# Kernel optimization log

Hardware: AMD Instinct MI355X
Metric: run time of the kernel (lower is better)

The kernel has to match this reference:

```python
import jax, jax.numpy as jnp
import numpy as np

N, M, D = 256, 1024, 512


def setup_inputs() -> dict:
    key = jax.random.key(0)
    ks = jax.random.split(key, 12)
    s = 1.0 / np.sqrt(D)
    return {
        "q": jax.random.normal(ks[0], (N, D), jnp.float32),
        "k": jax.random.normal(ks[1], (M, D), jnp.float32),
        "v": jax.random.normal(ks[2], (M, D), jnp.float32),
        "mask": jax.random.randint(ks[3], (N, M), 0, 2, jnp.int32),
        "WQ": jax.random.normal(ks[4], (D, D), jnp.float32) * s,
        "bQ": jax.random.normal(ks[5], (D,), jnp.float32) * s,
        "WK": jax.random.normal(ks[6], (D, D), jnp.float32) * s,
        "bK": jax.random.normal(ks[7], (D,), jnp.float32) * s,
        "WV": jax.random.normal(ks[8], (D, D), jnp.float32) * s,
        "bV": jax.random.normal(ks[9], (D,), jnp.float32) * s,
        "Ww": jax.random.normal(ks[10], (1, D), jnp.float32) * s,
        "bw": jax.random.normal(ks[11], (1,), jnp.float32) * s,
    }


def reference(q, k, v, mask, WQ, bQ, WK, bK, WV, bV, Ww, bw):
    # Linear projections (torch Linear: x @ W.T + b)
    qp = q @ WQ.T + bQ            # [N, D]
    kp = k @ WK.T + bK            # [M, D]
    vp = v @ WV.T + bV            # [M, D]
    # Additive (Bahdanau) scores: tanh(q_n + k_m) . w  -> [N, M]
    t = jnp.tanh(qp[:, None, :] + kp[None, :, :])   # [N, M, D]
    score = jnp.einsum("nmd,d->nm", t, Ww[0]) + bw[0]
    score = jnp.where(mask == 1, score, jnp.float32(-1e6))
    w = jax.nn.softmax(score, axis=1)               # softmax over keys (dim 1)
    context = jnp.einsum("nm,md->nd", w, vp)        # weighted sum over keys
    return context
```

## Files before the change

### kernel.cpp

```cpp
#include <hip/hip_runtime.h>

#define NQ 256
#define MK 1024
#define DD 512
#define CSC 2.8853900817779268f
#define L2E 1.4426950408889634f

typedef __attribute__((ext_vector_type(8))) short short8;
typedef __attribute__((ext_vector_type(4))) float floatx4;

__device__ inline void bsplit(float x, unsigned short& h, unsigned short& l)
{
    unsigned u = __float_as_uint(x);
    unsigned hr = (u + 0x7FFFu + ((u >> 16) & 1u)) >> 16;
    h = (unsigned short)hr;
    float hf = __uint_as_float(hr << 16);
    unsigned ul = __float_as_uint(x - hf);
    l = (unsigned short)((ul + 0x7FFFu + ((ul >> 16) & 1u)) >> 16);
}

__global__ __launch_bounds__(256) void convert_split(
    const float* __restrict__ q, const float* __restrict__ k, const float* __restrict__ v,
    const float* __restrict__ WQ, const float* __restrict__ WK, const float* __restrict__ WV,
    unsigned short* __restrict__ qhi, unsigned short* __restrict__ qlo,
    unsigned short* __restrict__ khi, unsigned short* __restrict__ klo,
    unsigned short* __restrict__ vhi, unsigned short* __restrict__ vlo,
    unsigned short* __restrict__ wqhi, unsigned short* __restrict__ wqlo,
    unsigned short* __restrict__ wkhi, unsigned short* __restrict__ wklo,
    unsigned short* __restrict__ wvhi, unsigned short* __restrict__ wvlo)
{
    const int i = blockIdx.x * 256 + threadIdx.x;
    const float* src; unsigned short *dh, *dl; int li;
    if (i < 32768)       { src = q;  dh = qhi;  dl = qlo;  li = i; }
    else if (i < 163840) { src = k;  dh = khi;  dl = klo;  li = i - 32768; }
    else if (i < 294912) { src = v;  dh = vhi;  dl = vlo;  li = i - 163840; }
    else if (i < 360448) { src = WQ; dh = wqhi; dl = wqlo; li = i - 294912; }
    else if (i < 425984) { src = WK; dh = wkhi; dl = wklo; li = i - 360448; }
    else                 { src = WV; dh = wvhi; dl = wvlo; li = i - 425984; }

    float4 x = *(const float4*)&src[li * 4];
    ushort4 h, l;
    bsplit(x.x, h.x, l.x); bsplit(x.y, h.y, l.y);
    bsplit(x.z, h.z, l.z); bsplit(x.w, h.w, l.w);
    *(ushort4*)&dh[li * 4] = h;
    *(ushort4*)&dl[li * 4] = l;
}

__global__ __launch_bounds__(256) void proj_mfma(
    const unsigned short* __restrict__ qhi, const unsigned short* __restrict__ qlo,
    const unsigned short* __restrict__ khi, const unsigned short* __restrict__ klo,
    const unsigned short* __restrict__ vhi, const unsigned short* __restrict__ vlo,
    const unsigned short* __restrict__ wqhi, const unsigned short* __restrict__ wqlo,
    const unsigned short* __restrict__ wkhi, const unsigned short* __restrict__ wklo,
    const unsigned short* __restrict__ wvhi, const unsigned short* __restrict__ wvlo,
    const float* __restrict__ bQ, const float* __restrict__ bK, const float* __restrict__ bV,
    float* __restrict__ qs, float* __restrict__ kts, float* __restrict__ vp)
{
    int t = blockIdx.x;
    const unsigned short *Xh, *Xl, *Wh, *Wl; const float* b; int mode;
    if (t < 32)       { mode = 0; Xh = qhi; Xl = qlo; Wh = wqhi; Wl = wqlo; b = bQ; }
    else if (t < 160) { mode = 1; t -= 32;  Xh = khi; Xl = klo; Wh = wkhi; Wl = wklo; b = bK; }
    else              { mode = 2; t -= 160; Xh = vhi; Xl = vlo; Wh = wvhi; Wl = wvlo; b = bV; }
    const int i0 = (t >> 3) * 64;
    const int j0 = (t & 7) * 64;

    const int l  = threadIdx.x & 63;
    const int w  = threadIdx.x >> 6;
    const int lr = l & 15;
    const int lk = (l >> 4) * 8;
    const int rbase = (l >> 4) * 4;

    const int arow = (i0 + w * 16 + lr) * DD;

    floatx4 acc[4] = {{0,0,0,0},{0,0,0,0},{0,0,0,0},{0,0,0,0}};

    for (int kk = 0; kk < DD; kk += 32) {
        short8 ah = *(const short8*)&Xh[arow + kk + lk];
        short8 al = *(const short8*)&Xl[arow + kk + lk];
#pragma unroll
        for (int nt = 0; nt < 4; ++nt) {
            const int brow = (j0 + nt * 16 + lr) * DD;
            short8 bh = *(const short8*)&Wh[brow + kk + lk];
            short8 bl = *(const short8*)&Wl[brow + kk + lk];
            acc[nt] = __builtin_amdgcn_mfma_f32_16x16x32_bf16(ah, bh, acc[nt], 0, 0, 0);
            acc[nt] = __builtin_amdgcn_mfma_f32_16x16x32_bf16(ah, bl, acc[nt], 0, 0, 0);
            acc[nt] = __builtin_amdgcn_mfma_f32_16x16x32_bf16(al, bh, acc[nt], 0, 0, 0);
        }
    }

    if (mode == 1) {
#pragma unroll
        for (int nt = 0; nt < 4; ++nt) {
            const float bb = b[j0 + nt * 16 + lr];
            float4 o;
            o.x = (acc[nt][0] + bb) * CSC;
            o.y = (acc[nt][1] + bb) * CSC;
            o.z = (acc[nt][2] + bb) * CSC;
            o.w = (acc[nt][3] + bb) * CSC;
            *(float4*)&kts[(j0 + nt * 16 + lr) * MK + i0 + w * 16 + rbase] = o;
        }
    } else {
        float* dst = (mode == 0) ? qs : vp;
        const float sc = (mode == 0) ? CSC : 1.0f;
#pragma unroll
        for (int nt = 0; nt < 4; ++nt) {
            const float bb = b[j0 + nt * 16 + lr];
#pragma unroll
            for (int j = 0; j < 4; ++j)
                dst[(i0 + w * 16 + rbase + j) * DD + j0 + nt * 16 + lr]
                    = (acc[nt][j] + bb) * sc;
        }
    }
}

__global__ __launch_bounds__(1024) void score_sm(
    const float* __restrict__ qs, const float* __restrict__ kts,
    const float* __restrict__ Ww, const int* __restrict__ mask,
    float* __restrict__ S)
{
    const int n = blockIdx.x;
    const int t = threadIdx.x;
    const int lane = t & 63, wave = t >> 6;

    __shared__ float qsm[DD];
    __shared__ float wwm[DD];
    __shared__ float red[16];

    if (t < DD) { qsm[t] = qs[n * DD + t]; wwm[t] = Ww[t]; }
    __syncthreads();

    float acc = 0.f;
    for (int d = 0; d < DD; d += 8) {
        float kv[8];
#pragma unroll
        for (int j = 0; j < 8; ++j) kv[j] = kts[(d + j) * MK + t];
#pragma unroll
        for (int j = 0; j < 8; ++j) {
            float x = qsm[d + j] + kv[j];
            float e = __builtin_amdgcn_exp2f(x);
            acc = fmaf(wwm[d + j], __builtin_amdgcn_rcpf(e + 1.0f), acc);
        }
    }

    float s = -2.0f * acc;
    s = (mask[n * MK + t] == 1) ? s : -1e6f;

    float mx = s;
    for (int o = 32; o > 0; o >>= 1) mx = fmaxf(mx, __shfl_xor(mx, o, 64));
    if (lane == 0) red[wave] = mx;
    __syncthreads();
    if (wave == 0) {
        float r = red[lane & 15];
        for (int o = 8; o > 0; o >>= 1) r = fmaxf(r, __shfl_xor(r, o, 64));
        if (lane == 0) red[0] = r;
    }
    __syncthreads();
    mx = red[0];
    __syncthreads();

    float e = __builtin_amdgcn_exp2f((s - mx) * L2E);
    float sum = e;
    for (int o = 32; o > 0; o >>= 1) sum += __shfl_xor(sum, o, 64);
    if (lane == 0) red[wave] = sum;
    __syncthreads();
    if (wave == 0) {
        float r = red[lane & 15];
        for (int o = 8; o > 0; o >>= 1) r += __shfl_xor(r, o, 64);
        if (lane == 0) red[0] = r;
    }
    __syncthreads();
    sum = red[0];

    S[n * MK + t] = e * __builtin_amdgcn_rcpf(sum);
}

#define CNG 8
#define CMC 256

__global__ __launch_bounds__(512) void context_v2(const float* __restrict__ S,
                                                  const float* __restrict__ vp,
                                                  float* __restrict__ out)
{
    __shared__ float ws[CMC][12];
    const int t = threadIdx.x;
    const int n0 = blockIdx.x * CNG;
    const int m0 = blockIdx.y * CMC;

#pragma unroll
    for (int p = 0; p < 4; ++p) {
        int e = t + p * 512;
        int m = e & 255, n = e >> 8;
        ws[m][n] = S[(n0 + n) * MK + m0 + m];
    }
    __syncthreads();

    float acc[CNG] = {};
    for (int m = 0; m < CMC; ++m) {
        float vv = vp[(m0 + m) * DD + t];
        float4 w0 = *(const float4*)&ws[m][0];
        float4 w4 = *(const float4*)&ws[m][4];
        acc[0] = fmaf(w0.x, vv, acc[0]);
        acc[1] = fmaf(w0.y, vv, acc[1]);
        acc[2] = fmaf(w0.z, vv, acc[2]);
        acc[3] = fmaf(w0.w, vv, acc[3]);
        acc[4] = fmaf(w4.x, vv, acc[4]);
        acc[5] = fmaf(w4.y, vv, acc[5]);
        acc[6] = fmaf(w4.z, vv, acc[6]);
        acc[7] = fmaf(w4.w, vv, acc[7]);
    }
#pragma unroll
    for (int n = 0; n < CNG; ++n) atomicAdd(&out[(n0 + n) * DD + t], acc[n]);
}

extern "C" void kernel_launch(void* const* d_in, const int* in_sizes, int n_in,
                              void* d_out, int out_size, void* d_ws, size_t ws_size,
                              hipStream_t stream)
{
    const float* q    = (const float*)d_in[0];
    const float* k    = (const float*)d_in[1];
    const float* v    = (const float*)d_in[2];
    const int*   mask = (const int*)  d_in[3];
    const float* WQ   = (const float*)d_in[4];
    const float* bQ   = (const float*)d_in[5];
    const float* WK   = (const float*)d_in[6];
    const float* bK   = (const float*)d_in[7];
    const float* WV   = (const float*)d_in[8];
    const float* bV   = (const float*)d_in[9];
    const float* Ww   = (const float*)d_in[10];
    const float* bw   = (const float*)d_in[11];
    (void)bw;
    float* out = (float*)d_out;

    float* qs  = (float*)d_ws;
    float* kts = qs + NQ * DD;
    float* vp  = kts + DD * MK;
    float* S   = vp + MK * DD;
    unsigned short* p16  = (unsigned short*)(S + NQ * MK);
    unsigned short* qhi  = p16;              p16 += NQ * DD;
    unsigned short* qlo  = p16;              p16 += NQ * DD;
    unsigned short* khi  = p16;              p16 += MK * DD;
    unsigned short* klo  = p16;              p16 += MK * DD;
    unsigned short* vhi  = p16;              p16 += MK * DD;
    unsigned short* vlo  = p16;              p16 += MK * DD;
    unsigned short* wqhi = p16;              p16 += DD * DD;
    unsigned short* wqlo = p16;              p16 += DD * DD;
    unsigned short* wkhi = p16;              p16 += DD * DD;
    unsigned short* wklo = p16;              p16 += DD * DD;
    unsigned short* wvhi = p16;              p16 += DD * DD;
    unsigned short* wvlo = p16;

    hipMemsetAsync(d_out, 0, (size_t)NQ * DD * sizeof(float), stream);

    convert_split<<<1920, 256, 0, stream>>>(q, k, v, WQ, WK, WV,
        qhi, qlo, khi, klo, vhi, vlo, wqhi, wqlo, wkhi, wklo, wvhi, wvlo);

    proj_mfma<<<288, 256, 0, stream>>>(qhi, qlo, khi, klo, vhi, vlo,
        wqhi, wqlo, wkhi, wklo, wvhi, wvlo, bQ, bK, bV, qs, kts, vp);

    score_sm<<<NQ, 1024, 0, stream>>>(qs, kts, Ww, mask, S);

    context_v2<<<dim3(NQ / CNG, MK / CMC), dim3(512), 0, stream>>>(S, vp, out);
}
```

Before: 177.6 us.

## Swizzle bf16 operand layout for MFMA and block-interleave projected keys

The conversion kernel now writes the bf16 hi/lo splits in a tiled, swizzled layout. Each wave's MFMA operand fetch becomes one contiguous 16-byte-per-lane load, replacing row-strided loads. The key projection is stored as [D/8][M][8] so the score kernel reads eight d-values per thread with two float4 loads, and q and Ww are interleaved in shared memory to be read as a float2. This targets poor coalescing in the projection GEMM and the score loop, at the cost of scattered 8-byte stores in the conversion kernel and in the key-projection epilogue.

Result: faster. 158.4 us (-10.8%).

```diff
diff --git a/kernel.cpp b/kernel.cpp
--- a/kernel.cpp
+++ b/kernel.cpp
@@ -8,6 +8,12 @@
 
 typedef __attribute__((ext_vector_type(8))) short short8;
 typedef __attribute__((ext_vector_type(4))) float floatx4;
+
+__device__ inline int swz(int i, int d)
+{
+    return (((i >> 4) * 16 + (d >> 5)) << 9) | (((d >> 3) & 3) << 7)
+         | ((i & 15) << 3) | (d & 7);
+}
 
 __device__ inline void bsplit(float x, unsigned short& h, unsigned short& l)
 {
@@ -29,21 +35,24 @@
     unsigned short* __restrict__ wkhi, unsigned short* __restrict__ wklo,
     unsigned short* __restrict__ wvhi, unsigned short* __restrict__ wvlo)
 {
-    const int i = blockIdx.x * 256 + threadIdx.x;
+    const int i4 = blockIdx.x * 256 + threadIdx.x;
     const float* src; unsigned short *dh, *dl; int li;
-    if (i < 32768)       { src = q;  dh = qhi;  dl = qlo;  li = i; }
-    else if (i < 163840) { src = k;  dh = khi;  dl = klo;  li = i - 32768; }
-    else if (i < 294912) { src = v;  dh = vhi;  dl = vlo;  li = i - 163840; }
-    else if (i < 360448) { src = WQ; dh = wqhi; dl = wqlo; li = i - 294912; }
-    else if (i < 425984) { src = WK; dh = wkhi; dl = wklo; li = i - 360448; }
-    else                 { src = WV; dh = wvhi; dl = wvlo; li = i - 425984; }
+    if (i4 < 32768)       { src = q;  dh = qhi;  dl = qlo;  li = i4; }
+    else if (i4 < 163840) { src = k;  dh = khi;  dl = klo;  li = i4 - 32768; }
+    else if (i4 < 294912) { src = v;  dh = vhi;  dl = vlo;  li = i4 - 163840; }
+    else if (i4 < 360448) { src = WQ; dh = wqhi; dl = wqlo; li = i4 - 294912; }
+    else if (i4 < 425984) { src = WK; dh = wkhi; dl = wklo; li = i4 - 360448; }
+    else                  { src = WV; dh = wvhi; dl = wvlo; li = i4 - 425984; }
 
     float4 x = *(const float4*)&src[li * 4];
     ushort4 h, l;
     bsplit(x.x, h.x, l.x); bsplit(x.y, h.y, l.y);
     bsplit(x.z, h.z, l.z); bsplit(x.w, h.w, l.w);
-    *(ushort4*)&dh[li * 4] = h;
-    *(ushort4*)&dl[li * 4] = l;
+
+    const int e = li * 4;
+    const int o = swz(e >> 9, e & 511);
+    *(ushort4*)&dh[o] = h;
+    *(ushort4*)&dl[o] = l;
 }
 
 __global__ __launch_bounds__(256) void proj_mfma(
@@ -67,21 +76,23 @@
     const int l  = threadIdx.x & 63;
     const int w  = threadIdx.x >> 6;
     const int lr = l & 15;
-    const int lk = (l >> 4) * 8;
     const int rbase = (l >> 4) * 4;
 
-    const int arow = (i0 + w * 16 + lr) * DD;
+    const unsigned short* Ah = Xh + ((i0 >> 4) + w) * 8192 + l * 8;
+    const unsigned short* Al = Xl + ((i0 >> 4) + w) * 8192 + l * 8;
+    const unsigned short* Bh = Wh + (j0 >> 4) * 8192 + l * 8;
+    const unsigned short* Bl = Wl + (j0 >> 4) * 8192 + l * 8;
 
     floatx4 acc[4] = {{0,0,0,0},{0,0,0,0},{0,0,0,0},{0,0,0,0}};
 
-    for (int kk = 0; kk < DD; kk += 32) {
-        short8 ah = *(const short8*)&Xh[arow + kk + lk];
-        short8 al = *(const short8*)&Xl[arow + kk + lk];
+#pragma unroll
+    for (int kc = 0; kc < 16; ++kc) {
+        short8 ah = *(const short8*)(Ah + kc * 512);
+        short8 al = *(const short8*)(Al + kc * 512);
 #pragma unroll
         for (int nt = 0; nt < 4; ++nt) {
-            const int brow = (j0 + nt * 16 + lr) * DD;
-            short8 bh = *(const short8*)&Wh[brow + kk + lk];
-            short8 bl = *(const short8*)&Wl[brow + kk + lk];
+            short8 bh = *(const short8*)(Bh + nt * 8192 + kc * 512);
+            short8 bl = *(const short8*)(Bl + nt * 8192 + kc * 512);
             acc[nt] = __builtin_amdgcn_mfma_f32_16x16x32_bf16(ah, bh, acc[nt], 0, 0, 0);
             acc[nt] = __builtin_amdgcn_mfma_f32_16x16x32_bf16(ah, bl, acc[nt], 0, 0, 0);
             acc[nt] = __builtin_amdgcn_mfma_f32_16x16x32_bf16(al, bh, acc[nt], 0, 0, 0);
@@ -91,13 +102,12 @@
     if (mode == 1) {
 #pragma unroll
         for (int nt = 0; nt < 4; ++nt) {
-            const float bb = b[j0 + nt * 16 + lr];
-            float4 o;
-            o.x = (acc[nt][0] + bb) * CSC;
-            o.y = (acc[nt][1] + bb) * CSC;
-            o.z = (acc[nt][2] + bb) * CSC;
-            o.w = (acc[nt][3] + bb) * CSC;
-            *(float4*)&kts[(j0 + nt * 16 + lr) * MK + i0 + w * 16 + rbase] = o;
+            const int d = j0 + nt * 16 + lr;
+            const float bb = b[d];
+            float* base = &kts[(((d >> 3) * MK) + i0 + w * 16 + rbase) * 8 + (d & 7)];
+#pragma unroll
+            for (int j = 0; j < 4; ++j)
+                base[j * 8] = (acc[nt][j] + bb) * CSC;
         }
     } else {
         float* dst = (mode == 0) ? qs : vp;
@@ -122,23 +132,23 @@
     const int t = threadIdx.x;
     const int lane = t & 63, wave = t >> 6;
 
-    __shared__ float qsm[DD];
-    __shared__ float wwm[DD];
+    __shared__ float qw[DD * 2];
     __shared__ float red[16];
 
-    if (t < DD) { qsm[t] = qs[n * DD + t]; wwm[t] = Ww[t]; }
-    __syncthreads();
-
+    if (t < DD) { qw[t * 2] = qs[n * DD + t]; qw[t * 2 + 1] = Ww[t]; }
+    __syncthreads();
+
+    const float* kp = kts + t * 8;
     float acc = 0.f;
-    for (int d = 0; d < DD; d += 8) {
-        float kv[8];
-#pragma unroll
-        for (int j = 0; j < 8; ++j) kv[j] = kts[(d + j) * MK + t];
+    for (int c = 0; c < 64; ++c) {
+        float4 k0 = *(const float4*)(kp + c * (MK * 8));
+        float4 k1 = *(const float4*)(kp + c * (MK * 8) + 4);
+        float kv[8] = {k0.x, k0.y, k0.z, k0.w, k1.x, k1.y, k1.z, k1.w};
 #pragma unroll
         for (int j = 0; j < 8; ++j) {
-            float x = qsm[d + j] + kv[j];
-            float e = __builtin_amdgcn_exp2f(x);
-            acc = fmaf(wwm[d + j], __builtin_amdgcn_rcpf(e + 1.0f), acc);
+            float2 wq = *(const float2*)&qw[(c * 8 + j) * 2];
+            float e = __builtin_amdgcn_exp2f(wq.x + kv[j]);
+            acc = fmaf(wq.y, __builtin_amdgcn_rcpf(e + 1.0f), acc);
         }
     }
 
```
